# Optimization experiments

Measured on AMD Instinct MI355X. Metric: run time of the kernel, lower is better.

Reference implementation:

```python
import jax, jax.numpy as jnp
import numpy as np

B, S, D, H = 4, 2048, 1024, 16
HD = D // H
SCALE = D ** (-0.5)  # NOTE: original scales by embedding_dim**-0.5, not head_size**-0.5


def setup_inputs() -> dict:
    key = jax.random.key(0)
    k1, k2, k3, k4, k5 = jax.random.split(key, 5)
    return {
        "x": jax.random.normal(k1, (B, S, D), dtype=jnp.float32),
        "Wqkv": jax.random.normal(k2, (3 * D, D), dtype=jnp.float32) * (D ** -0.5),
        "bqkv": jax.random.normal(k3, (3 * D,), dtype=jnp.float32) * 0.02,
        "Wlift": jax.random.normal(k4, (D, D), dtype=jnp.float32) * (D ** -0.5),
        "blift": jax.random.normal(k5, (D,), dtype=jnp.float32) * 0.02,
    }


def reference(x, Wqkv, bqkv, Wlift, blift):
    b, s, d = x.shape
    # qkv projection -> (b, s, 3, H, HD) -> (3, b, H, s, HD)
    qkv = (x @ Wqkv.T + bqkv).reshape(b, s, 3, H, HD).transpose(2, 0, 3, 1, 4)
    q, k, v = qkv[0], qkv[1], qkv[2]  # each (b, H, s, HD)
    # full score matrix, softmax over keys
    scores = jnp.einsum("bhqd,bhkd->bhqk", q, k) * SCALE
    a = jax.nn.softmax(scores, axis=-1)
    # post-hoc causal mask + renormalize (as in the original)
    a = jnp.tril(a)
    a = a / jnp.sum(a, axis=-1, keepdims=True)
    attn = jnp.einsum("bhqk,bhkd->bhqd", a, v)  # (b, H, s, HD)
    attn = attn.swapaxes(1, 2).reshape(b, s, d)  # (b, s, d)
    # lifting linear; Dropout(0.2) is identity in eval mode
    return attn @ Wlift.T + blift
```

## Files before the change

### kernel.cpp

```cpp
#include <hip/hip_runtime.h>
#include <cstdint>
#include <cstddef>

typedef unsigned short u16;
typedef unsigned int u32;
typedef __bf16 bf16x8 __attribute__((ext_vector_type(8)));
typedef float f32x4 __attribute__((ext_vector_type(4)));
typedef float f32x16 __attribute__((ext_vector_type(16)));

__device__ __forceinline__ u16 f2bf(float f) {
  unsigned u = __builtin_bit_cast(unsigned, f);
  return (u16)((u + 0x7FFFu + ((u >> 16) & 1u)) >> 16);
}

__device__ __forceinline__ u32 pk2bf(float lo, float hi) {
  union { __bf16 h[2]; u32 u; } t;
  t.h[0] = (__bf16)lo; t.h[1] = (__bf16)hi;
  return t.u;
}

__device__ __forceinline__ void gl_lds16(const void* g, void* l) {
  __builtin_amdgcn_global_load_lds(
      (const __attribute__((address_space(1))) unsigned int*)g,
      (__attribute__((address_space(3))) unsigned int*)l,
      16, 0, 0);
}

__global__ void cast4_kernel(const float* __restrict__ in, u16* __restrict__ out, int n4) {
  int i = blockIdx.x * blockDim.x + threadIdx.x;
  if (i < n4) {
    float4 v = reinterpret_cast<const float4*>(in)[i];
    ushort4 o;
    o.x = f2bf(v.x); o.y = f2bf(v.y); o.z = f2bf(v.z); o.w = f2bf(v.w);
    reinterpret_cast<ushort4*>(out)[i] = o;
  }
}

template <int EPI>
__global__ __launch_bounds__(256)
void gemm_bt_kernel(const u16* __restrict__ A, const u16* __restrict__ Bw,
                    const float* __restrict__ bias,
                    u16* __restrict__ oq, u16* __restrict__ ok, u16* __restrict__ ovT,
                    float* __restrict__ ofp, int M, int N, int K) {
  __shared__ __align__(16) u16 Als[2][128 * 32];
  __shared__ __align__(16) u16 Bls[2][128 * 32];

  const int tid = threadIdx.x;
  const int lane = tid & 63;
  const int w = tid >> 6, wr = w >> 1, wc = w & 1;
  const int lr = lane & 15, lk = lane >> 4;
  const int brow = blockIdx.y * 128, bcol = blockIdx.x * 128;

  const int srow = tid >> 2;
  const int scol = (tid & 3) << 3;
  const u16* ga = A + (size_t)(brow + srow) * K + scol;
  const u16* gb = Bw + (size_t)(bcol + srow) * K + scol;

  f32x4 acc[4][4] = {};

  auto stage = [&](int buf, int kt) {
    const u16* a0 = ga + kt * 32;
    const u16* b0 = gb + kt * 32;
    gl_lds16(a0,             &Als[buf][tid * 8]);
    gl_lds16(a0 + 64 * K,    &Als[buf][2048 + tid * 8]);
    gl_lds16(b0,             &Bls[buf][tid * 8]);
    gl_lds16(b0 + 64 * K,    &Bls[buf][2048 + tid * 8]);
  };

  stage(0, 0);
  __syncthreads();

  const int nt = K >> 5;
  int cur = 0;
  for (int t = 0; t < nt; ++t) {
    if (t + 1 < nt) stage(cur ^ 1, t + 1);
    bf16x8 af[4], bfr[4];
#pragma unroll
    for (int m = 0; m < 4; ++m)
      af[m] = *reinterpret_cast<const bf16x8*>(&Als[cur][(wr * 64 + m * 16 + lr) * 32 + lk * 8]);
#pragma unroll
    for (int n = 0; n < 4; ++n)
      bfr[n] = *reinterpret_cast<const bf16x8*>(&Bls[cur][(wc * 64 + n * 16 + lr) * 32 + lk * 8]);
#pragma unroll
    for (int m = 0; m < 4; ++m)
#pragma unroll
      for (int n = 0; n < 4; ++n)
        acc[m][n] = __builtin_amdgcn_mfma_f32_16x16x32_bf16(af[m], bfr[n], acc[m][n], 0, 0, 0);
    __syncthreads();
    cur ^= 1;
  }

  if (EPI == 0) {
    const int three = bcol >> 10;
#pragma unroll
    for (int n = 0; n < 4; ++n) {
      const int c = bcol + wc * 64 + n * 16 + lr;
      const float bv = bias[c];
      const int cc = c & 1023, h = cc >> 6, hd = cc & 63;
#pragma unroll
      for (int m = 0; m < 4; ++m) {
        const int r0 = brow + wr * 64 + m * 16 + lk * 4;
        const int b = r0 >> 11;
        const int s0 = r0 & 2047;
        if (three == 2) {
          ushort4 pkv;
          pkv.x = f2bf(acc[m][n][0] + bv);
          pkv.y = f2bf(acc[m][n][1] + bv);
          pkv.z = f2bf(acc[m][n][2] + bv);
          pkv.w = f2bf(acc[m][n][3] + bv);
          *reinterpret_cast<ushort4*>(&ovT[((size_t)(b * 16 + h) * 64 + hd) * 2048 + s0]) = pkv;
        } else {
          u16* dst = (three == 0) ? oq : ok;
          const float sc = (three == 0) ? 0.03125f * 1.44269504089f : 1.0f;
#pragma unroll
          for (int j = 0; j < 4; ++j)
            dst[((size_t)(b * 16 + h) * 2048 + (s0 + j)) * 64 + hd] = f2bf((acc[m][n][j] + bv) * sc);
        }
      }
    }
  } else {
#pragma unroll
    for (int n = 0; n < 4; ++n) {
      const int c = bcol + wc * 64 + n * 16 + lr;
      const float bv = bias[c];
#pragma unroll
      for (int m = 0; m < 4; ++m) {
        const int r0 = brow + wr * 64 + m * 16 + lk * 4;
#pragma unroll
        for (int j = 0; j < 4; ++j)
          ofp[(size_t)(r0 + j) * N + c] = acc[m][n][j] + bv;
      }
    }
  }
}

__global__ __launch_bounds__(256)
void attn_causal_kernel(const u16* __restrict__ qg, const u16* __restrict__ kg_,
                        const u16* __restrict__ vT, u16* __restrict__ ob) {
  __shared__ __align__(16) u16 Kls[2][64 * 64];
  __shared__ __align__(16) u16 Vls[2][64 * 64];

  const int tid = threadIdx.x, lane = tid & 63, w = tid >> 6;
  const int n = lane & 31, hi = lane >> 5;
  const int bid = blockIdx.x;
  const int qbi = 15 - (bid >> 6);
  const int bh = bid & 63;
  const int q0w = qbi * 128 + w * 32;
  const size_t base = (size_t)bh * 2048 * 64;
  const size_t vbase = (size_t)bh * 64 * 2048;

  bf16x8 qf[4];
#pragma unroll
  for (int dc = 0; dc < 4; ++dc)
    qf[dc] = *reinterpret_cast<const bf16x8*>(
        &qg[base + (size_t)(q0w + n) * 64 + dc * 16 + hi * 8]);

  f32x16 o0 = {}, o1 = {};
  float l = 0.f;

  const int ktiles = qbi * 2 + 2;

  const int krow = tid >> 3, kch = tid & 7;

  auto stage = [&](int buf, int t) {
    const int k0 = t << 6;
#pragma unroll
    for (int p = 0; p < 2; ++p) {
      const int r = p * 32 + krow;
      const int sz = (r ^ (r >> 3)) & 7;
      gl_lds16(kg_ + base + (size_t)(k0 + r) * 64 + (kch ^ sz) * 8,
               &Kls[buf][p * 2048 + tid * 8]);
      gl_lds16(vT + vbase + (size_t)r * 2048 + k0 + (kch ^ sz) * 8,
               &Vls[buf][p * 2048 + tid * 8]);
    }
  };

  const int swk0 = ((n ^ (n >> 3)) & 7) << 4;
  const int swk1 = (((32 + n) ^ ((32 + n) >> 3)) & 7) << 4;
  const int swv0 = swk0;
  const int swv1 = swk1;

  stage(0, 0);
  __syncthreads();

  int cur = 0;
  for (int t = 0; t < ktiles; ++t) {
    const int k0 = t << 6;
    if (t + 1 < ktiles) stage(cur ^ 1, t + 1);
    const char* Kb = (const char*)&Kls[cur][0];
    const char* Vb = (const char*)&Vls[cur][0];
#pragma unroll
    for (int mt = 0; mt < 2; ++mt) {
      const int kb0 = k0 + mt * 32;
      if (kb0 <= q0w + 31) {
        f32x16 st = {};
        const int swk = mt ? swk1 : swk0;
#pragma unroll
        for (int dc = 0; dc < 4; ++dc) {
          bf16x8 kf = *reinterpret_cast<const bf16x8*>(
              Kb + (mt * 32 + n) * 128 + ((((dc << 1) | hi) << 4) ^ swk));
          st = __builtin_amdgcn_mfma_f32_32x32x16_bf16(kf, qf[dc], st, 0, 0, 0);
        }
        if (kb0 == q0w) {
#pragma unroll
          for (int r = 0; r < 16; ++r) {
            const int koff = (r & 3) + 8 * (r >> 2) + 4 * hi;
            if (koff > n) st[r] = -1e30f;
          }
        }
        float rs = 0.f;
#pragma unroll
        for (int r = 0; r < 16; ++r) {
          st[r] = __builtin_amdgcn_exp2f(st[r]);
          rs += st[r];
        }
        l += rs;
#pragma unroll
        for (int kk = 0; kk < 2; ++kk) {
          const int gown = (kk * 2 + hi) * 4, gsnd = (kk * 2 + (hi ^ 1)) * 4;
          u32 a0 = pk2bf(st[gown + 0], st[gown + 1]);
          u32 a1 = pk2bf(st[gown + 2], st[gown + 3]);
          u32 s0 = pk2bf(st[gsnd + 0], st[gsnd + 1]);
          u32 s1 = pk2bf(st[gsnd + 2], st[gsnd + 3]);
          u32 rA = __shfl_xor(s0, 32, 64);
          u32 rB = __shfl_xor(s1, 32, 64);
          union { u32 u[4]; bf16x8 v; } pb;
          pb.u[0] = hi ? rA : a0;
          pb.u[1] = hi ? rB : a1;
          pb.u[2] = hi ? a0 : rA;
          pb.u[3] = hi ? a1 : rB;
          const int c = ((mt * 4 + kk * 2 + hi) << 4);
          bf16x8 vf0 = *reinterpret_cast<const bf16x8*>(Vb + n * 128 + (c ^ swv0));
          o0 = __builtin_amdgcn_mfma_f32_32x32x16_bf16(vf0, pb.v, o0, 0, 0, 0);
          bf16x8 vf1 = *reinterpret_cast<const bf16x8*>(Vb + (32 + n) * 128 + (c ^ swv1));
          o1 = __builtin_amdgcn_mfma_f32_32x32x16_bf16(vf1, pb.v, o1, 0, 0, 0);
        }
      }
    }
    __syncthreads();
    cur ^= 1;
  }

  const int b = bh >> 4, h = bh & 15;
  const float lt = l + __shfl_xor(l, 32, 64);
  const float inv = 1.f / lt;
  const size_t rbase = ((size_t)(b * 2048 + q0w + n)) * 1024 + h * 64;
#pragma unroll
  for (int g = 0; g < 4; ++g) {
    ushort4 w0, w1;
    w0.x = f2bf(o0[g * 4 + 0] * inv); w0.y = f2bf(o0[g * 4 + 1] * inv);
    w0.z = f2bf(o0[g * 4 + 2] * inv); w0.w = f2bf(o0[g * 4 + 3] * inv);
    w1.x = f2bf(o1[g * 4 + 0] * inv); w1.y = f2bf(o1[g * 4 + 1] * inv);
    w1.z = f2bf(o1[g * 4 + 2] * inv); w1.w = f2bf(o1[g * 4 + 3] * inv);
    *reinterpret_cast<ushort4*>(&ob[rbase + g * 8 + hi * 4]) = w0;
    *reinterpret_cast<ushort4*>(&ob[rbase + 32 + g * 8 + hi * 4]) = w1;
  }
}

extern "C" void kernel_launch(void* const* d_in, const int* in_sizes, int n_in,
                              void* d_out, int out_size, void* d_ws, size_t ws_size,
                              hipStream_t stream) {
  const float* x     = (const float*)d_in[0];
  const float* Wqkv  = (const float*)d_in[1];
  const float* bqkv  = (const float*)d_in[2];
  const float* Wlift = (const float*)d_in[3];
  const float* blift = (const float*)d_in[4];
  float* out = (float*)d_out;

  if (ws_size < 40ull * 1024 * 1024) return;

  char* ws = (char*)d_ws;
  u16* xb     = (u16*)(ws);
  u16* wqkvb  = (u16*)(ws + 16777216);
  u16* wliftb = (u16*)(ws + 23068672);
  u16* vT     = (u16*)(ws + 25165824);
  u16* attnb  = xb;
  u16* qb = (u16*)d_out;
  u16* kb = qb + 8388608;

  cast4_kernel<<<8192, 256, 0, stream>>>(x, xb, 2097152);
  cast4_kernel<<<3072, 256, 0, stream>>>(Wqkv, wqkvb, 786432);
  cast4_kernel<<<1024, 256, 0, stream>>>(Wlift, wliftb, 262144);

  gemm_bt_kernel<0><<<dim3(24, 64), 256, 0, stream>>>(
      xb, wqkvb, bqkv, qb, kb, vT, nullptr, 8192, 3072, 1024);

  attn_causal_kernel<<<1024, 256, 0, stream>>>(qb, kb, vT, attnb);

  gemm_bt_kernel<1><<<dim3(8, 64), 256, 0, stream>>>(
      attnb, wliftb, blift, nullptr, nullptr, nullptr, out, 8192, 1024, 1024);
}
```

Before: 268.9 us.

## Pre-tile K/V into MFMA fragment layout and load directly to registers in attention

The QKV GEMM epilogue now writes K and V in a blocked layout where each 32-key slab matches the MFMA operand fragment order. The attention kernel drops its LDS staging and barriers, loading K and V fragments straight from global memory into registers with a double-buffered K prefetch. Each wave now processes only the slabs it needs (per-wave causal bound), and blocks are remapped so each XCD works on a subset of heads with a balanced query-block order. It also adds s_setprio around MFMAs and a launch_bounds occupancy hint. The cost is that blocks no longer share K/V through LDS, so each wave issues its own global loads and relies on cache for reuse.

```diff
diff --git a/kernel.cpp b/kernel.cpp
--- a/kernel.cpp
+++ b/kernel.cpp
@@ -102,19 +102,29 @@
         const int r0 = brow + wr * 64 + m * 16 + lk * 4;
         const int b = r0 >> 11;
         const int s0 = r0 & 2047;
+        const size_t bh131 = (size_t)(b * 16 + h) * 131072;
         if (three == 2) {
           ushort4 pkv;
           pkv.x = f2bf(acc[m][n][0] + bv);
           pkv.y = f2bf(acc[m][n][1] + bv);
           pkv.z = f2bf(acc[m][n][2] + bv);
           pkv.w = f2bf(acc[m][n][3] + bv);
-          *reinterpret_cast<ushort4*>(&ovT[((size_t)(b * 16 + h) * 64 + hd) * 2048 + s0]) = pkv;
+          const size_t addr = bh131 + (size_t)(s0 >> 5) * 2048 +
+                              (size_t)(((hd >> 5) * 2) + ((s0 >> 4) & 1)) * 512 +
+                              (hd & 31) * 16 + (s0 & 15);
+          *reinterpret_cast<ushort4*>(&ovT[addr]) = pkv;
+        } else if (three == 1) {
+#pragma unroll
+          for (int j = 0; j < 4; ++j) {
+            const int s = s0 + j;
+            ok[bh131 + (size_t)(s >> 5) * 2048 + (hd >> 4) * 512 +
+               (s & 31) * 16 + (hd & 15)] = f2bf(acc[m][n][j] + bv);
+          }
         } else {
-          u16* dst = (three == 0) ? oq : ok;
-          const float sc = (three == 0) ? 0.03125f * 1.44269504089f : 1.0f;
+          const float sc = 0.03125f * 1.44269504089f;
 #pragma unroll
           for (int j = 0; j < 4; ++j)
-            dst[((size_t)(b * 16 + h) * 2048 + (s0 + j)) * 64 + hd] = f2bf((acc[m][n][j] + bv) * sc);
+            oq[((size_t)(b * 16 + h) * 2048 + (s0 + j)) * 64 + hd] = f2bf((acc[m][n][j] + bv) * sc);
         }
       }
     }
@@ -134,111 +144,95 @@
   }
 }
 
-__global__ __launch_bounds__(256)
-void attn_causal_kernel(const u16* __restrict__ qg, const u16* __restrict__ kg_,
-                        const u16* __restrict__ vT, u16* __restrict__ ob) {
-  __shared__ __align__(16) u16 Kls[2][64 * 64];
-  __shared__ __align__(16) u16 Vls[2][64 * 64];
-
+__global__ __launch_bounds__(256, 4)
+void attn_causal_kernel(const u16* __restrict__ qg, const u16* __restrict__ k5,
+                        const u16* __restrict__ v5, u16* __restrict__ ob) {
   const int tid = threadIdx.x, lane = tid & 63, w = tid >> 6;
   const int n = lane & 31, hi = lane >> 5;
   const int bid = blockIdx.x;
-  const int qbi = 15 - (bid >> 6);
-  const int bh = bid & 63;
+  const int xcd = bid & 7, idx = bid >> 3;
+  const int bh = (xcd << 3) | (idx & 7);
+  const int a = idx >> 3, a0 = a & 3, kq = a >> 2;
+  int qbi;
+  if (kq == 0) qbi = 15 - a0;
+  else if (kq == 1) qbi = 8 + (a0 ^ 2);
+  else if (kq == 2) qbi = 4 + a0;
+  else qbi = a0 ^ 1;
   const int q0w = qbi * 128 + w * 32;
-  const size_t base = (size_t)bh * 2048 * 64;
-  const size_t vbase = (size_t)bh * 64 * 2048;
+
+  const u16* Kb = k5 + (size_t)bh * 131072;
+  const u16* Vb = v5 + (size_t)bh * 131072;
+  const int lanep = n * 16 + hi * 8;
 
   bf16x8 qf[4];
+  const size_t qbase = (size_t)bh * 131072 + (size_t)(q0w + n) * 64 + hi * 8;
 #pragma unroll
   for (int dc = 0; dc < 4; ++dc)
-    qf[dc] = *reinterpret_cast<const bf16x8*>(
-        &qg[base + (size_t)(q0w + n) * 64 + dc * 16 + hi * 8]);
+    qf[dc] = *reinterpret_cast<const bf16x8*>(&qg[qbase + dc * 16]);
 
   f32x16 o0 = {}, o1 = {};
   float l = 0.f;
-
-  const int ktiles = qbi * 2 + 2;
-
-  const int krow = tid >> 3, kch = tid & 7;
-
-  auto stage = [&](int buf, int t) {
-    const int k0 = t << 6;
-#pragma unroll
-    for (int p = 0; p < 2; ++p) {
-      const int r = p * 32 + krow;
-      const int sz = (r ^ (r >> 3)) & 7;
-      gl_lds16(kg_ + base + (size_t)(k0 + r) * 64 + (kch ^ sz) * 8,
-               &Kls[buf][p * 2048 + tid * 8]);
-      gl_lds16(vT + vbase + (size_t)r * 2048 + k0 + (kch ^ sz) * 8,
-               &Vls[buf][p * 2048 + tid * 8]);
+  const int nslabs = qbi * 4 + w + 1;
+
+  bf16x8 kfA[4], kfB[4];
+#pragma unroll
+  for (int dc = 0; dc < 4; ++dc)
+    kfA[dc] = *reinterpret_cast<const bf16x8*>(&Kb[dc * 512 + lanep]);
+
+  auto body = [&](int t, bf16x8 (&kc)[4], bf16x8 (&kn)[4]) {
+    bf16x8 vf[4];
+#pragma unroll
+    for (int c = 0; c < 4; ++c)
+      vf[c] = *reinterpret_cast<const bf16x8*>(&Vb[(size_t)t * 2048 + c * 512 + lanep]);
+    if (t + 1 < nslabs) {
+#pragma unroll
+      for (int dc = 0; dc < 4; ++dc)
+        kn[dc] = *reinterpret_cast<const bf16x8*>(&Kb[(size_t)(t + 1) * 2048 + dc * 512 + lanep]);
+    }
+    __builtin_amdgcn_s_setprio(1);
+    f32x16 st = {};
+#pragma unroll
+    for (int dc = 0; dc < 4; ++dc)
+      st = __builtin_amdgcn_mfma_f32_32x32x16_bf16(kc[dc], qf[dc], st, 0, 0, 0);
+    __builtin_amdgcn_s_setprio(0);
+    if (t == nslabs - 1) {
+#pragma unroll
+      for (int r = 0; r < 16; ++r) {
+        const int koff = (r & 3) + 8 * (r >> 2) + 4 * hi;
+        if (koff > n) st[r] = -1e30f;
+      }
+    }
+    float rs = 0.f;
+#pragma unroll
+    for (int r = 0; r < 16; ++r) { st[r] = __builtin_amdgcn_exp2f(st[r]); rs += st[r]; }
+    l += rs;
+#pragma unroll
+    for (int kk = 0; kk < 2; ++kk) {
+      const int gown = (kk * 2 + hi) * 4, gsnd = (kk * 2 + (hi ^ 1)) * 4;
+      u32 pa0 = pk2bf(st[gown + 0], st[gown + 1]);
+      u32 pa1 = pk2bf(st[gown + 2], st[gown + 3]);
+      u32 ps0 = pk2bf(st[gsnd + 0], st[gsnd + 1]);
+      u32 ps1 = pk2bf(st[gsnd + 2], st[gsnd + 3]);
+      u32 rA = __shfl_xor(ps0, 32, 64);
+      u32 rB = __shfl_xor(ps1, 32, 64);
+      union { u32 u[4]; bf16x8 v; } pb;
+      pb.u[0] = hi ? rA : pa0;
+      pb.u[1] = hi ? rB : pa1;
+      pb.u[2] = hi ? pa0 : rA;
+      pb.u[3] = hi ? pa1 : rB;
+      __builtin_amdgcn_s_setprio(1);
+      o0 = __builtin_amdgcn_mfma_f32_32x32x16_bf16(vf[kk],     pb.v, o0, 0, 0, 0);
+      o1 = __builtin_amdgcn_mfma_f32_32x32x16_bf16(vf[2 + kk], pb.v, o1, 0, 0, 0);
+      __builtin_amdgcn_s_setprio(0);
     }
   };
 
-  const int swk0 = ((n ^ (n >> 3)) & 7) << 4;
-  const int swk1 = (((32 + n) ^ ((32 + n) >> 3)) & 7) << 4;
-  const int swv0 = swk0;
-  const int swv1 = swk1;
-
-  stage(0, 0);
-  __syncthreads();
-
-  int cur = 0;
-  for (int t = 0; t < ktiles; ++t) {
-    const int k0 = t << 6;
-    if (t + 1 < ktiles) stage(cur ^ 1, t + 1);
-    const char* Kb = (const char*)&Kls[cur][0];
-    const char* Vb = (const char*)&Vls[cur][0];
-#pragma unroll
-    for (int mt = 0; mt < 2; ++mt) {
-      const int kb0 = k0 + mt * 32;
-      if (kb0 <= q0w + 31) {
-        f32x16 st = {};
-        const int swk = mt ? swk1 : swk0;
-#pragma unroll
-        for (int dc = 0; dc < 4; ++dc) {
-          bf16x8 kf = *reinterpret_cast<const bf16x8*>(
-              Kb + (mt * 32 + n) * 128 + ((((dc << 1) | hi) << 4) ^ swk));
-          st = __builtin_amdgcn_mfma_f32_32x32x16_bf16(kf, qf[dc], st, 0, 0, 0);
-        }
-        if (kb0 == q0w) {
-#pragma unroll
-          for (int r = 0; r < 16; ++r) {
-            const int koff = (r & 3) + 8 * (r >> 2) + 4 * hi;
-            if (koff > n) st[r] = -1e30f;
-          }
-        }
-        float rs = 0.f;
-#pragma unroll
-        for (int r = 0; r < 16; ++r) {
-          st[r] = __builtin_amdgcn_exp2f(st[r]);
-          rs += st[r];
-        }
-        l += rs;
-#pragma unroll
-        for (int kk = 0; kk < 2; ++kk) {
-          const int gown = (kk * 2 + hi) * 4, gsnd = (kk * 2 + (hi ^ 1)) * 4;
-          u32 a0 = pk2bf(st[gown + 0], st[gown + 1]);
-          u32 a1 = pk2bf(st[gown + 2], st[gown + 3]);
-          u32 s0 = pk2bf(st[gsnd + 0], st[gsnd + 1]);
-          u32 s1 = pk2bf(st[gsnd + 2], st[gsnd + 3]);
-          u32 rA = __shfl_xor(s0, 32, 64);
-          u32 rB = __shfl_xor(s1, 32, 64);
-          union { u32 u[4]; bf16x8 v; } pb;
-          pb.u[0] = hi ? rA : a0;
-          pb.u[1] = hi ? rB : a1;
-          pb.u[2] = hi ? a0 : rA;
-          pb.u[3] = hi ? a1 : rB;
-          const int c = ((mt * 4 + kk * 2 + hi) << 4);
-          bf16x8 vf0 = *reinterpret_cast<const bf16x8*>(Vb + n * 128 + (c ^ swv0));
-          o0 = __builtin_amdgcn_mfma_f32_32x32x16_bf16(vf0, pb.v, o0, 0, 0, 0);
-          bf16x8 vf1 = *reinterpret_cast<const bf16x8*>(Vb + (32 + n) * 128 + (c ^ swv1));
-          o1 = __builtin_amdgcn_mfma_f32_32x32x16_bf16(vf1, pb.v, o1, 0, 0, 0);
-        }
-      }
-    }
-    __syncthreads();
-    cur ^= 1;
+  int t = 0;
+  for (;;) {
+    body(t, kfA, kfB);
+    if (++t >= nslabs) break;
+    body(t, kfB, kfA);
+    if (++t >= nslabs) break;
   }
 
   const int b = bh >> 4, h = bh & 15;
@@ -273,19 +267,19 @@
   u16* xb     = (u16*)(ws);
   u16* wqkvb  = (u16*)(ws + 16777216);
   u16* wliftb = (u16*)(ws + 23068672);
-  u16* vT     = (u16*)(ws + 25165824);
+  u16* v5     = (u16*)(ws + 25165824);
   u16* attnb  = xb;
   u16* qb = (u16*)d_out;
-  u16* kb = qb + 8388608;
+  u16* k5 = qb + 8388608;
 
   cast4_kernel<<<8192, 256, 0, stream>>>(x, xb, 2097152);
   cast4_kernel<<<3072, 256, 0, stream>>>(Wqkv, wqkvb, 786432);
   cast4_kernel<<<1024, 256, 0, stream>>>(Wlift, wliftb, 262144);
 
   gemm_bt_kernel<0><<<dim3(24, 64), 256, 0, stream>>>(
-      xb, wqkvb, bqkv, qb, kb, vT, nullptr, 8192, 3072, 1024);
-
-  attn_causal_kernel<<<1024, 256, 0, stream>>>(qb, kb, vT, attnb);
+      xb, wqkvb, bqkv, qb, k5, v5, nullptr, 8192, 3072, 1024);
+
+  attn_causal_kernel<<<1024, 256, 0, stream>>>(qb, k5, v5, attnb);
 
   gemm_bt_kernel<1><<<dim3(8, 64), 256, 0, stream>>>(
       attnb, wliftb, blift, nullptr, nullptr, nullptr, out, 8192, 1024, 1024);
```

Result: slower. 309.6 us (+15.2%).

## Enlarge attention blocks to 512 threads and batch score MFMAs with priority hints

Applied to the files above, without the earlier changes.

The attention kernel now runs 8 waves per block covering 256 query rows, so each staged 64-key K/V tile is reused by twice as many waves. With 512 threads the staging needs one load per thread per tile, and the block order is reshuffled to balance causal work. Inside each tile both 32-key score MFMAs are issued back to back before the softmax, and the P·V MFMAs are grouped into a separate phase. Those MFMA phases are wrapped in s_setprio to favour matrix issue across waves. In exchange each block holds twice the LDS consumers, has more register pressure under launch_bounds(512,4), and syncs across more waves per tile.

```diff
diff --git a/kernel.cpp b/kernel.cpp
--- a/kernel.cpp
+++ b/kernel.cpp
@@ -134,7 +134,7 @@
   }
 }
 
-__global__ __launch_bounds__(256)
+__global__ __launch_bounds__(512, 4)
 void attn_causal_kernel(const u16* __restrict__ qg, const u16* __restrict__ kg_,
                         const u16* __restrict__ vT, u16* __restrict__ ob) {
   __shared__ __align__(16) u16 Kls[2][64 * 64];
@@ -143,9 +143,9 @@
   const int tid = threadIdx.x, lane = tid & 63, w = tid >> 6;
   const int n = lane & 31, hi = lane >> 5;
   const int bid = blockIdx.x;
-  const int qbi = 15 - (bid >> 6);
   const int bh = bid & 63;
-  const int q0w = qbi * 128 + w * 32;
+  const int qb = (bid < 256) ? (7 - (bid >> 6)) : ((bid - 256) >> 6);
+  const int q0w = qb * 256 + w * 32;
   const size_t base = (size_t)bh * 2048 * 64;
   const size_t vbase = (size_t)bh * 64 * 2048;
 
@@ -158,27 +158,20 @@
   f32x16 o0 = {}, o1 = {};
   float l = 0.f;
 
-  const int ktiles = qbi * 2 + 2;
+  const int ktiles = qb * 4 + 4;
 
   const int krow = tid >> 3, kch = tid & 7;
+  const int szr = (krow ^ (krow >> 3)) & 7;
+  const u16* kgp = kg_ + base + (size_t)krow * 64 + (kch ^ szr) * 8;
+  const u16* vgp = vT + vbase + (size_t)krow * 2048 + (kch ^ szr) * 8;
 
   auto stage = [&](int buf, int t) {
-    const int k0 = t << 6;
-#pragma unroll
-    for (int p = 0; p < 2; ++p) {
-      const int r = p * 32 + krow;
-      const int sz = (r ^ (r >> 3)) & 7;
-      gl_lds16(kg_ + base + (size_t)(k0 + r) * 64 + (kch ^ sz) * 8,
-               &Kls[buf][p * 2048 + tid * 8]);
-      gl_lds16(vT + vbase + (size_t)r * 2048 + k0 + (kch ^ sz) * 8,
-               &Vls[buf][p * 2048 + tid * 8]);
-    }
+    gl_lds16(kgp + (size_t)t * 4096, &Kls[buf][tid * 8]);
+    gl_lds16(vgp + t * 64,           &Vls[buf][tid * 8]);
   };
 
-  const int swk0 = ((n ^ (n >> 3)) & 7) << 4;
-  const int swk1 = (((32 + n) ^ ((32 + n) >> 3)) & 7) << 4;
-  const int swv0 = swk0;
-  const int swv1 = swk1;
+  const int sw0 = ((n ^ (n >> 3)) & 7) << 4;
+  const int sw1 = (((32 + n) ^ ((32 + n) >> 3)) & 7) << 4;
 
   stage(0, 0);
   __syncthreads();
@@ -187,55 +180,87 @@
   for (int t = 0; t < ktiles; ++t) {
     const int k0 = t << 6;
     if (t + 1 < ktiles) stage(cur ^ 1, t + 1);
-    const char* Kb = (const char*)&Kls[cur][0];
-    const char* Vb = (const char*)&Vls[cur][0];
-#pragma unroll
-    for (int mt = 0; mt < 2; ++mt) {
-      const int kb0 = k0 + mt * 32;
-      if (kb0 <= q0w + 31) {
-        f32x16 st = {};
-        const int swk = mt ? swk1 : swk0;
+    if (k0 <= q0w) {
+      const char* Kb = (const char*)&Kls[cur][0];
+      const char* Vb = (const char*)&Vls[cur][0];
+      const bool act1 = (k0 + 32) <= q0w;
+
+      f32x16 st0 = {}, st1 = {};
+      __builtin_amdgcn_s_setprio(1);
+#pragma unroll
+      for (int dc = 0; dc < 4; ++dc) {
+        bf16x8 kf = *reinterpret_cast<const bf16x8*>(
+            Kb + n * 128 + ((((dc << 1) | hi) << 4) ^ sw0));
+        st0 = __builtin_amdgcn_mfma_f32_32x32x16_bf16(kf, qf[dc], st0, 0, 0, 0);
+      }
+      if (act1) {
 #pragma unroll
         for (int dc = 0; dc < 4; ++dc) {
           bf16x8 kf = *reinterpret_cast<const bf16x8*>(
-              Kb + (mt * 32 + n) * 128 + ((((dc << 1) | hi) << 4) ^ swk));
-          st = __builtin_amdgcn_mfma_f32_32x32x16_bf16(kf, qf[dc], st, 0, 0, 0);
-        }
-        if (kb0 == q0w) {
-#pragma unroll
-          for (int r = 0; r < 16; ++r) {
-            const int koff = (r & 3) + 8 * (r >> 2) + 4 * hi;
-            if (koff > n) st[r] = -1e30f;
-          }
-        }
-        float rs = 0.f;
+              Kb + (32 + n) * 128 + ((((dc << 1) | hi) << 4) ^ sw1));
+          st1 = __builtin_amdgcn_mfma_f32_32x32x16_bf16(kf, qf[dc], st1, 0, 0, 0);
+        }
+      }
+      __builtin_amdgcn_s_setprio(0);
+
+      if (k0 == q0w) {
 #pragma unroll
         for (int r = 0; r < 16; ++r) {
-          st[r] = __builtin_amdgcn_exp2f(st[r]);
-          rs += st[r];
-        }
-        l += rs;
+          const int koff = (r & 3) + 8 * (r >> 2) + 4 * hi;
+          if (koff > n) st0[r] = -1e30f;
+        }
+      }
+      if (act1 && (k0 + 32) == q0w) {
+#pragma unroll
+        for (int r = 0; r < 16; ++r) {
+          const int koff = (r & 3) + 8 * (r >> 2) + 4 * hi;
+          if (koff > n) st1[r] = -1e30f;
+        }
+      }
+
+      float rs = 0.f;
+#pragma unroll
+      for (int r = 0; r < 16; ++r) { st0[r] = __builtin_amdgcn_exp2f(st0[r]); rs += st0[r]; }
+      if (act1) {
+#pragma unroll
+        for (int r = 0; r < 16; ++r) { st1[r] = __builtin_amdgcn_exp2f(st1[r]); rs += st1[r]; }
+      }
+      l += rs;
+
+      union { u32 u[4]; bf16x8 v; } pb[4];
+#pragma unroll
+      for (int s = 0; s < 2; ++s) {
+        if (s == 1 && !act1) break;
+        const f32x16& st = s ? st1 : st0;
 #pragma unroll
         for (int kk = 0; kk < 2; ++kk) {
           const int gown = (kk * 2 + hi) * 4, gsnd = (kk * 2 + (hi ^ 1)) * 4;
-          u32 a0 = pk2bf(st[gown + 0], st[gown + 1]);
-          u32 a1 = pk2bf(st[gown + 2], st[gown + 3]);
-          u32 s0 = pk2bf(st[gsnd + 0], st[gsnd + 1]);
-          u32 s1 = pk2bf(st[gsnd + 2], st[gsnd + 3]);
-          u32 rA = __shfl_xor(s0, 32, 64);
-          u32 rB = __shfl_xor(s1, 32, 64);
-          union { u32 u[4]; bf16x8 v; } pb;
-          pb.u[0] = hi ? rA : a0;
-          pb.u[1] = hi ? rB : a1;
-          pb.u[2] = hi ? a0 : rA;
-          pb.u[3] = hi ? a1 : rB;
-          const int c = ((mt * 4 + kk * 2 + hi) << 4);
-          bf16x8 vf0 = *reinterpret_cast<const bf16x8*>(Vb + n * 128 + (c ^ swv0));
-          o0 = __builtin_amdgcn_mfma_f32_32x32x16_bf16(vf0, pb.v, o0, 0, 0, 0);
-          bf16x8 vf1 = *reinterpret_cast<const bf16x8*>(Vb + (32 + n) * 128 + (c ^ swv1));
-          o1 = __builtin_amdgcn_mfma_f32_32x32x16_bf16(vf1, pb.v, o1, 0, 0, 0);
-        }
-      }
+          u32 pa0 = pk2bf(st[gown + 0], st[gown + 1]);
+          u32 pa1 = pk2bf(st[gown + 2], st[gown + 3]);
+          u32 ps0 = pk2bf(st[gsnd + 0], st[gsnd + 1]);
+          u32 ps1 = pk2bf(st[gsnd + 2], st[gsnd + 3]);
+          u32 rA = __shfl_xor(ps0, 32, 64);
+          u32 rB = __shfl_xor(ps1, 32, 64);
+          pb[s * 2 + kk].u[0] = hi ? rA : pa0;
+          pb[s * 2 + kk].u[1] = hi ? rB : pa1;
+          pb[s * 2 + kk].u[2] = hi ? pa0 : rA;
+          pb[s * 2 + kk].u[3] = hi ? pa1 : rB;
+        }
+      }
+      __builtin_amdgcn_s_setprio(1);
+#pragma unroll
+      for (int s = 0; s < 2; ++s) {
+        if (s == 1 && !act1) break;
+#pragma unroll
+        for (int kk = 0; kk < 2; ++kk) {
+          const int c = ((s * 4 + kk * 2 + hi) << 4);
+          bf16x8 vf0 = *reinterpret_cast<const bf16x8*>(Vb + n * 128 + (c ^ sw0));
+          o0 = __builtin_amdgcn_mfma_f32_32x32x16_bf16(vf0, pb[s * 2 + kk].v, o0, 0, 0, 0);
+          bf16x8 vf1 = *reinterpret_cast<const bf16x8*>(Vb + (32 + n) * 128 + (c ^ sw1));
+          o1 = __builtin_amdgcn_mfma_f32_32x32x16_bf16(vf1, pb[s * 2 + kk].v, o1, 0, 0, 0);
+        }
+      }
+      __builtin_amdgcn_s_setprio(0);
     }
     __syncthreads();
     cur ^= 1;
@@ -285,7 +310,7 @@
   gemm_bt_kernel<0><<<dim3(24, 64), 256, 0, stream>>>(
       xb, wqkvb, bqkv, qb, kb, vT, nullptr, 8192, 3072, 1024);
 
-  attn_causal_kernel<<<1024, 256, 0, stream>>>(qb, kb, vT, attnb);
+  attn_causal_kernel<<<512, 512, 0, stream>>>(qb, kb, vT, attnb);
 
   gemm_bt_kernel<1><<<dim3(8, 64), 256, 0, stream>>>(
       attnb, wliftb, blift, nullptr, nullptr, nullptr, out, 8192, 1024, 1024);
```

After: 299.8 us. +11.5%, slower.

## Shrink attention blocks to two waves with 32-key tiles and MFMA priority hints

Applied to the files above, without the earlier changes.

Restructures the causal attention kernel so each block has 2 waves over 64 queries instead of 4 waves over 128, and streams 32-key K/V tiles with a new swizzle. Blocks double to 2048 and launch bounds now request higher occupancy. The aim is better load balance over the causal triangle, finer-grained causal skipping, and more resident blocks per CU. s_setprio hints are added around the MFMA sections. In exchange, each K/V tile is reused by fewer queries, so global/LDS traffic per FLOP rises and there are more barrier iterations.

```diff
diff --git a/kernel.cpp b/kernel.cpp
--- a/kernel.cpp
+++ b/kernel.cpp
@@ -134,18 +134,19 @@
   }
 }
 
-__global__ __launch_bounds__(256)
+__global__ __launch_bounds__(128, 4)
 void attn_causal_kernel(const u16* __restrict__ qg, const u16* __restrict__ kg_,
                         const u16* __restrict__ vT, u16* __restrict__ ob) {
-  __shared__ __align__(16) u16 Kls[2][64 * 64];
-  __shared__ __align__(16) u16 Vls[2][64 * 64];
+  __shared__ __align__(16) u16 Kls[2][32 * 64];
+  __shared__ __align__(16) u16 Vls[2][64 * 32];
 
   const int tid = threadIdx.x, lane = tid & 63, w = tid >> 6;
   const int n = lane & 31, hi = lane >> 5;
   const int bid = blockIdx.x;
-  const int qbi = 15 - (bid >> 6);
   const int bh = bid & 63;
-  const int q0w = qbi * 128 + w * 32;
+  const int qb = 31 - (bid >> 6);
+  const int q0w = qb * 64 + w * 32;
+  const int jdiag = 2 * qb + w;
   const size_t base = (size_t)bh * 2048 * 64;
   const size_t vbase = (size_t)bh * 64 * 2048;
 
@@ -158,83 +159,84 @@
   f32x16 o0 = {}, o1 = {};
   float l = 0.f;
 
-  const int ktiles = qbi * 2 + 2;
-
-  const int krow = tid >> 3, kch = tid & 7;
+  const int ktiles = 2 * qb + 2;
+
+  const int lct = tid & 63;
+  const int rK0 = w * 16 + (lct >> 3), cK = lct & 7;
+  const int rV0 = w * 32 + (lct >> 2), cV = lct & 3;
+  const u16* kgp0 = kg_ + base + (size_t)rK0 * 64 + ((cK ^ ((rK0 ^ (rK0 >> 3)) & 7)) * 8);
+  const u16* kgp1 = kg_ + base + (size_t)(rK0 + 8) * 64 + ((cK ^ (((rK0 + 8) ^ ((rK0 + 8) >> 3)) & 7)) * 8);
+  const u16* vgp0 = vT + vbase + (size_t)rV0 * 2048 + ((cV ^ ((rV0 ^ (rV0 >> 2)) & 3)) * 8);
+  const u16* vgp1 = vT + vbase + (size_t)(rV0 + 16) * 2048 + ((cV ^ (((rV0 + 16) ^ ((rV0 + 16) >> 2)) & 3)) * 8);
+  const int dK = tid * 8 + w * 512;
+  const int dV = tid * 8 + w * 512;
 
   auto stage = [&](int buf, int t) {
-    const int k0 = t << 6;
-#pragma unroll
-    for (int p = 0; p < 2; ++p) {
-      const int r = p * 32 + krow;
-      const int sz = (r ^ (r >> 3)) & 7;
-      gl_lds16(kg_ + base + (size_t)(k0 + r) * 64 + (kch ^ sz) * 8,
-               &Kls[buf][p * 2048 + tid * 8]);
-      gl_lds16(vT + vbase + (size_t)r * 2048 + k0 + (kch ^ sz) * 8,
-               &Vls[buf][p * 2048 + tid * 8]);
-    }
+    const size_t ko = (size_t)t * 2048;
+    gl_lds16(kgp0 + ko, &Kls[buf][dK]);
+    gl_lds16(kgp1 + ko, &Kls[buf][dK + 512]);
+    gl_lds16(vgp0 + t * 32, &Vls[buf][dV]);
+    gl_lds16(vgp1 + t * 32, &Vls[buf][dV + 512]);
   };
 
-  const int swk0 = ((n ^ (n >> 3)) & 7) << 4;
-  const int swk1 = (((32 + n) ^ ((32 + n) >> 3)) & 7) << 4;
-  const int swv0 = swk0;
-  const int swv1 = swk1;
+  const int swk = ((n ^ (n >> 3)) & 7) << 4;
+  const int sv0 = ((n ^ (n >> 2)) & 3) << 4;
+  const int sv1 = (((32 + n) ^ ((32 + n) >> 2)) & 3) << 4;
 
   stage(0, 0);
   __syncthreads();
 
   int cur = 0;
   for (int t = 0; t < ktiles; ++t) {
-    const int k0 = t << 6;
     if (t + 1 < ktiles) stage(cur ^ 1, t + 1);
-    const char* Kb = (const char*)&Kls[cur][0];
-    const char* Vb = (const char*)&Vls[cur][0];
-#pragma unroll
-    for (int mt = 0; mt < 2; ++mt) {
-      const int kb0 = k0 + mt * 32;
-      if (kb0 <= q0w + 31) {
-        f32x16 st = {};
-        const int swk = mt ? swk1 : swk0;
-#pragma unroll
-        for (int dc = 0; dc < 4; ++dc) {
-          bf16x8 kf = *reinterpret_cast<const bf16x8*>(
-              Kb + (mt * 32 + n) * 128 + ((((dc << 1) | hi) << 4) ^ swk));
-          st = __builtin_amdgcn_mfma_f32_32x32x16_bf16(kf, qf[dc], st, 0, 0, 0);
+    if (t <= jdiag) {
+      const char* Kb = (const char*)&Kls[cur][0];
+      const char* Vb = (const char*)&Vls[cur][0];
+
+      f32x16 st = {};
+      __builtin_amdgcn_s_setprio(1);
+#pragma unroll
+      for (int dc = 0; dc < 4; ++dc) {
+        bf16x8 kf = *reinterpret_cast<const bf16x8*>(
+            Kb + n * 128 + ((((dc << 1) | hi) << 4) ^ swk));
+        st = __builtin_amdgcn_mfma_f32_32x32x16_bf16(kf, qf[dc], st, 0, 0, 0);
+      }
+      __builtin_amdgcn_s_setprio(0);
+
+      if (t == jdiag) {
+#pragma unroll
+        for (int r = 0; r < 16; ++r) {
+          const int koff = (r & 3) + 8 * (r >> 2) + 4 * hi;
+          if (koff > n) st[r] = -1e30f;
         }
-        if (kb0 == q0w) {
-#pragma unroll
-          for (int r = 0; r < 16; ++r) {
-            const int koff = (r & 3) + 8 * (r >> 2) + 4 * hi;
-            if (koff > n) st[r] = -1e30f;
-          }
-        }
-        float rs = 0.f;
-#pragma unroll
-        for (int r = 0; r < 16; ++r) {
-          st[r] = __builtin_amdgcn_exp2f(st[r]);
-          rs += st[r];
-        }
-        l += rs;
-#pragma unroll
-        for (int kk = 0; kk < 2; ++kk) {
-          const int gown = (kk * 2 + hi) * 4, gsnd = (kk * 2 + (hi ^ 1)) * 4;
-          u32 a0 = pk2bf(st[gown + 0], st[gown + 1]);
-          u32 a1 = pk2bf(st[gown + 2], st[gown + 3]);
-          u32 s0 = pk2bf(st[gsnd + 0], st[gsnd + 1]);
-          u32 s1 = pk2bf(st[gsnd + 2], st[gsnd + 3]);
-          u32 rA = __shfl_xor(s0, 32, 64);
-          u32 rB = __shfl_xor(s1, 32, 64);
-          union { u32 u[4]; bf16x8 v; } pb;
-          pb.u[0] = hi ? rA : a0;
-          pb.u[1] = hi ? rB : a1;
-          pb.u[2] = hi ? a0 : rA;
-          pb.u[3] = hi ? a1 : rB;
-          const int c = ((mt * 4 + kk * 2 + hi) << 4);
-          bf16x8 vf0 = *reinterpret_cast<const bf16x8*>(Vb + n * 128 + (c ^ swv0));
-          o0 = __builtin_amdgcn_mfma_f32_32x32x16_bf16(vf0, pb.v, o0, 0, 0, 0);
-          bf16x8 vf1 = *reinterpret_cast<const bf16x8*>(Vb + (32 + n) * 128 + (c ^ swv1));
-          o1 = __builtin_amdgcn_mfma_f32_32x32x16_bf16(vf1, pb.v, o1, 0, 0, 0);
-        }
+      }
+
+      float rs = 0.f;
+#pragma unroll
+      for (int r = 0; r < 16; ++r) { st[r] = __builtin_amdgcn_exp2f(st[r]); rs += st[r]; }
+      l += rs;
+
+#pragma unroll
+      for (int kk = 0; kk < 2; ++kk) {
+        const int gown = (kk * 2 + hi) * 4, gsnd = (kk * 2 + (hi ^ 1)) * 4;
+        u32 pa0 = pk2bf(st[gown + 0], st[gown + 1]);
+        u32 pa1 = pk2bf(st[gown + 2], st[gown + 3]);
+        u32 ps0 = pk2bf(st[gsnd + 0], st[gsnd + 1]);
+        u32 ps1 = pk2bf(st[gsnd + 2], st[gsnd + 3]);
+        u32 rA = __shfl_xor(ps0, 32, 64);
+        u32 rB = __shfl_xor(ps1, 32, 64);
+        union { u32 u[4]; bf16x8 v; } pb;
+        pb.u[0] = hi ? rA : pa0;
+        pb.u[1] = hi ? rB : pa1;
+        pb.u[2] = hi ? pa0 : rA;
+        pb.u[3] = hi ? pa1 : rB;
+        const int c = ((kk * 2 + hi) << 4);
+        __builtin_amdgcn_s_setprio(1);
+        bf16x8 vf0 = *reinterpret_cast<const bf16x8*>(Vb + n * 64 + (c ^ sv0));
+        o0 = __builtin_amdgcn_mfma_f32_32x32x16_bf16(vf0, pb.v, o0, 0, 0, 0);
+        bf16x8 vf1 = *reinterpret_cast<const bf16x8*>(Vb + (32 + n) * 64 + (c ^ sv1));
+        o1 = __builtin_amdgcn_mfma_f32_32x32x16_bf16(vf1, pb.v, o1, 0, 0, 0);
+        __builtin_amdgcn_s_setprio(0);
       }
     }
     __syncthreads();
@@ -285,7 +287,7 @@
   gemm_bt_kernel<0><<<dim3(24, 64), 256, 0, stream>>>(
       xb, wqkvb, bqkv, qb, kb, vT, nullptr, 8192, 3072, 1024);
 
-  attn_causal_kernel<<<1024, 256, 0, stream>>>(qb, kb, vT, attnb);
+  attn_causal_kernel<<<2048, 128, 0, stream>>>(qb, kb, vT, attnb);
 
   gemm_bt_kernel<1><<<dim3(8, 64), 256, 0, stream>>>(
       attnb, wliftb, blift, nullptr, nullptr, nullptr, out, 8192, 1024, 1024);
```

After: 301.4 us. 12.1% more time.
